# Optimization experiments

Measured on AMD Instinct MI355X. Metric: run time of the kernel, lower is better.

The kernel has to match this reference:

```python
import jax, jax.numpy as jnp
import numpy as np

OUT_F, IN_F = 4096, 4096
TOKENS = 8192


def setup_inputs() -> dict:
    key = jax.random.key(0)
    k0, k1, k2, k3 = jax.random.split(key, 4)
    CORE_SCALE = 0.05  # keep reconstructed W finite and well below the 1e6 sanity bound
    x = jax.random.normal(k0, (TOKENS, IN_F), dtype=jnp.float32)
    core0 = jax.random.normal(k1, (1, 16, 16, 64), dtype=jnp.float32) * CORE_SCALE
    core1 = jax.random.normal(k2, (64, 16, 16, 64), dtype=jnp.float32) * CORE_SCALE
    core2 = jax.random.normal(k3, (64, 16, 16, 1), dtype=jnp.float32) * CORE_SCALE
    return {"x": x, "core0": core0, "core1": core1, "core2": core2}


def _build_weight(cores):
    # Chain tensordot over bond dims: cores[k] is [r_{k-1}, o_k, i_k, r_k]
    t = cores[0].astype(jnp.float32)
    for c in cores[1:]:
        t = jnp.tensordot(t, c.astype(jnp.float32), axes=((-1,), (0,)))
    # squeeze the boundary bonds (both 1 for open boundary)
    t = t[0, ..., 0]  # shape [o1, i1, o2, i2, o3, i3]
    num = len(cores)
    # order 'oi': all o-axes first, then all i-axes (matches _contract_4d_chain_with)
    perm = list(range(0, 2 * num, 2)) + list(range(1, 2 * num, 2))
    t = jnp.transpose(t, perm)
    W = t.reshape(OUT_F, IN_F)
    # _clean_finite: nan/inf -> 0 (identity on finite values)
    return jnp.nan_to_num(W, nan=0.0, posinf=0.0, neginf=0.0)


def reference(x, core0, core1, core2):
    W = _build_weight([core0, core1, core2])  # [out_f, in_f], fp32
    # dense path: y = x @ W^T (nn.Linear semantics, no bias)
    return jnp.matmul(x, W.T)
```

## Files before the change

kernel.cpp:

```cpp
#include <hip/hip_runtime.h>

typedef __attribute__((ext_vector_type(8))) short  s8v;
typedef __attribute__((ext_vector_type(8))) unsigned short us8;
typedef __attribute__((ext_vector_type(4))) unsigned short us4;
typedef __attribute__((ext_vector_type(4))) float  f4v;

__device__ __forceinline__ unsigned short f2bf(float f) {
  unsigned int u = __builtin_bit_cast(unsigned int, f);
  u += 0x7fffu + ((u >> 16) & 1u);
  return (unsigned short)(u >> 16);
}

__device__ __forceinline__ void gll16(const void* g, void* l) {
  __builtin_amdgcn_global_load_lds(
      (const __attribute__((address_space(1))) unsigned int*)g,
      (__attribute__((address_space(3))) unsigned int*)l, 16, 0, 0);
}

__global__ __launch_bounds__(256) void cast_bf16(const float* __restrict__ in,
                                                 unsigned short* __restrict__ out) {
  const size_t i = (size_t)blockIdx.x * 256 + threadIdx.x;
  const f4v* p = (const f4v*)in;
  f4v a = p[2 * i];
  f4v b = p[2 * i + 1];
  us8 r;
  r[0] = f2bf(a[0]); r[1] = f2bf(a[1]); r[2] = f2bf(a[2]); r[3] = f2bf(a[3]);
  r[4] = f2bf(b[0]); r[5] = f2bf(b[1]); r[6] = f2bf(b[2]); r[7] = f2bf(b[3]);
  *(us8*)&out[i * 8] = r;
}

__global__ __launch_bounds__(256) void contract1b(const float* __restrict__ c0,
                                                  const float* __restrict__ c1,
                                                  unsigned short* __restrict__ T) {
  const int idx = blockIdx.x * 256 + threadIdx.x;
  const int r2q = idx & 15;
  const int oi2 = (idx >> 4) & 255;
  const int oi1 = idx >> 12;
  const float* c0p = c0 + oi1 * 64;
  const float* c1p = c1 + oi2 * 64 + r2q * 4;
  f4v s = (f4v)0.f;
#pragma unroll 8
  for (int r1 = 0; r1 < 64; ++r1) {
    const float t = c0p[r1];
    const f4v v = *(const f4v*)(c1p + r1 * 16384);
    s[0] = fmaf(t, v[0], s[0]); s[1] = fmaf(t, v[1], s[1]);
    s[2] = fmaf(t, v[2], s[2]); s[3] = fmaf(t, v[3], s[3]);
  }
  us4 o;
  o[0] = f2bf(s[0]); o[1] = f2bf(s[1]); o[2] = f2bf(s[2]); o[3] = f2bf(s[3]);
  *(us4*)&T[(size_t)idx * 4] = o;
}

__global__ __launch_bounds__(256) void transc2(const float* __restrict__ c2,
                                               unsigned short* __restrict__ c2t) {
  const int n = blockIdx.x * 16 + (threadIdx.x >> 4);
  const int j = threadIdx.x & 15;
  us4 o;
#pragma unroll
  for (int q = 0; q < 4; ++q) o[q] = f2bf(c2[(j * 4 + q) * 256 + n]);
  *(us4*)&c2t[(size_t)n * 64 + j * 4] = o;
}

__global__ __launch_bounds__(256) void buildW3(const unsigned short* __restrict__ T,
                                               const unsigned short* __restrict__ c2t,
                                               unsigned short* __restrict__ W) {
  __shared__ unsigned short sT[16384];
  __shared__ unsigned short sC[16384];

  const int tid = threadIdx.x;
  const int o1 = blockIdx.x >> 4, o2 = blockIdx.x & 15;

#pragma unroll
  for (int j = 0; j < 8; ++j) {
    const int c = j * 256 + tid;
    const int m = c >> 3, sl = c & 7;
    const int dst = m * 64 + ((sl ^ (m & 7)) << 3);
    *(us8*)&sT[dst] = *(const us8*)(T + (size_t)(o1 * 16 + (m >> 4)) * 16384 +
                                    (o2 * 16 + (m & 15)) * 64 + sl * 8);
    *(us8*)&sC[dst] = *(const us8*)(c2t + (size_t)m * 64 + sl * 8);
  }
  __syncthreads();

  const int lane = tid & 63, wid = tid >> 6;
  const int fr = lane & 15, ks = lane >> 4;
  const int f7 = fr & 7;
  const int sx0 = ((ks ^ f7) << 3);
  const int sx1 = (((4 + ks) ^ f7) << 3);

  s8v a[4][2];
#pragma unroll
  for (int mi = 0; mi < 4; ++mi) {
    const unsigned short* p = &sT[(wid * 64 + mi * 16 + fr) * 64];
    a[mi][0] = *(const s8v*)(p + sx0);
    a[mi][1] = *(const s8v*)(p + sx1);
  }
#pragma unroll
  for (int nt = 0; nt < 16; ++nt) {
    const unsigned short* p = &sC[(nt * 16 + fr) * 64];
    const s8v b0 = *(const s8v*)(p + sx0);
    const s8v b1 = *(const s8v*)(p + sx1);
#pragma unroll
    for (int mi = 0; mi < 4; ++mi) {
      f4v acc = (f4v)0.f;
      acc = __builtin_amdgcn_mfma_f32_16x16x32_bf16(a[mi][0], b0, acc, 0, 0, 0);
      acc = __builtin_amdgcn_mfma_f32_16x16x32_bf16(a[mi][1], b1, acc, 0, 0, 0);
      unsigned short* wp = W + (size_t)(o1 * 256 + o2 * 16 + nt) * 4096 +
                           (wid * 4 + mi) * 256 + fr;
#pragma unroll
      for (int r = 0; r < 4; ++r) wp[(ks * 4 + r) * 16] = f2bf(acc[r]);
    }
  }
}


#define SBAR() do { asm volatile("" ::: "memory"); __builtin_amdgcn_s_barrier(); asm volatile("" ::: "memory"); } while (0)
#define VMW(N) asm volatile("s_waitcnt vmcnt(" #N ")" ::: "memory")

template<int MQ, int NQ>
__device__ __forceinline__ void mmq(f4v (&acc)[8][4], const s8v (&a)[4][2], const s8v (&b)[2][2]) {
  __builtin_amdgcn_s_setprio(1);
#pragma unroll
  for (int mi = 0; mi < 4; ++mi)
#pragma unroll
    for (int ni = 0; ni < 2; ++ni)
#pragma unroll
      for (int q = 0; q < 2; ++q)
        acc[MQ * 4 + mi][NQ * 2 + ni] = __builtin_amdgcn_mfma_f32_16x16x32_bf16(
            a[mi][q], b[ni][q], acc[MQ * 4 + mi][NQ * 2 + ni], 0, 0, 0);
  __builtin_amdgcn_s_setprio(0);
}

__global__ __launch_bounds__(512, 2) void gemm8(const unsigned short* __restrict__ A,
                                                const unsigned short* __restrict__ B,
                                                float* __restrict__ C) {
  constexpr int N = 4096, K = 4096;
  constexpr int NT = K / 64;
  constexpr int NITER = NT / 2;
  constexpr int NXT = N / 256;

  __shared__ unsigned short lds[65536];

  const int tid  = threadIdx.x;
  const int lane = tid & 63;
  const int wid  = tid >> 6;
  const int wm   = wid >> 2;
  const int wn   = wid & 3;

  const int cpx = (int)gridDim.x >> 3;
  const int wg  = ((int)blockIdx.x & 7) * cpx + ((int)blockIdx.x >> 3);
  const long bm = (long)(wg / NXT) * 256;
  const long bn = (long)(wg % NXT) * 256;

  const int srow = tid >> 3;
  const int scol = ((tid & 7) ^ (srow & 7)) * 8;
  const unsigned short* gA = A + (bm + srow) * (size_t)K + scol;
  const unsigned short* gB = B + (bn + srow) * (size_t)K + scol;
  const size_t half64 = 64 * (size_t)K;
  const size_t k128   = 128 * (size_t)K;

#define STG(gp, koff, ldsU) do {                                  \
    const unsigned short* g_ = (gp) + (koff);                     \
    gll16(g_,          &lds[(ldsU) + tid * 8]);                   \
    gll16(g_ + half64, &lds[(ldsU) + 4096 + tid * 8]);            \
  } while (0)

  const int fr = lane & 15;
  const int ks = lane >> 4;
  const int f7 = fr & 7;
  const int sx0 = (ks ^ f7) * 8;
  const int sx1 = ((ks | 4) ^ f7) * 8;
  const int arow = (wm * 64 + fr) * 64;
  const int brow = (wn * 32 + fr) * 64;

#define RDA(MQ, bufU) do {                                                   \
    const unsigned short* p_ = &lds[(bufU) + (MQ) * 8192 + arow];            \
    a[0][0] = *(const s8v*)(p_ + sx0);        a[0][1] = *(const s8v*)(p_ + sx1); \
    a[1][0] = *(const s8v*)(p_ + 1024 + sx0); a[1][1] = *(const s8v*)(p_ + 1024 + sx1); \
    a[2][0] = *(const s8v*)(p_ + 2048 + sx0); a[2][1] = *(const s8v*)(p_ + 2048 + sx1); \
    a[3][0] = *(const s8v*)(p_ + 3072 + sx0); a[3][1] = *(const s8v*)(p_ + 3072 + sx1); \
  } while (0)
#define RDB(dst, NQ, bufU) do {                                              \
    const unsigned short* p_ = &lds[(bufU) + 16384 + (NQ) * 8192 + brow];    \
    dst[0][0] = *(const s8v*)(p_ + sx0);        dst[0][1] = *(const s8v*)(p_ + sx1); \
    dst[1][0] = *(const s8v*)(p_ + 1024 + sx0); dst[1][1] = *(const s8v*)(p_ + 1024 + sx1); \
  } while (0)

  f4v acc[8][4];
#pragma unroll
  for (int m = 0; m < 8; ++m)
#pragma unroll
    for (int n = 0; n < 4; ++n) acc[m][n] = (f4v)0.0f;

  STG(gA,        0, 0);
  STG(gA + k128, 0, 8192);
  STG(gB,        0, 16384);
  STG(gB + k128, 0, 24576);
  STG(gA,        64, 32768);
  VMW(2);
  SBAR();

  s8v a[4][2], bL[2][2], bH[2][2];

  for (int i = 0; i < NITER; ++i) {
    const long w46 = (i == NITER - 1) ? -128L : 0L;
    const long w8  = (i == NITER - 1) ? -192L : 0L;
    RDA(0, 0); RDB(bL, 0, 0); RDB(bH, 1, 0);
    STG(gB, 64, 32768 + 16384);
    SBAR(); mmq<0, 0>(acc, a, bL);
    STG(gA + k128, 64, 32768 + 8192);
    STG(gB + k128, 64, 32768 + 24576);
    SBAR(); mmq<0, 1>(acc, a, bH);
    RDA(1, 0);
    SBAR(); mmq<1, 0>(acc, a, bL);
    STG(gA, 128 + w46, 0);
    SBAR(); mmq<1, 1>(acc, a, bH);
    VMW(2); SBAR();
    RDA(0, 32768); RDB(bL, 0, 32768); RDB(bH, 1, 32768);
    STG(gB, 128 + w46, 16384);
    SBAR(); mmq<0, 0>(acc, a, bL);
    STG(gA + k128, 128 + w46, 8192);
    STG(gB + k128, 128 + w46, 24576);
    SBAR(); mmq<0, 1>(acc, a, bH);
    RDA(1, 32768);
    SBAR(); mmq<1, 0>(acc, a, bL);
    STG(gA, 192 + w8, 32768);
    SBAR(); mmq<1, 1>(acc, a, bH);
    VMW(2); SBAR();

    gA += 128; gB += 128;
  }
  VMW(0);

#pragma unroll
  for (int mq = 0; mq < 2; ++mq)
#pragma unroll
    for (int mi = 0; mi < 4; ++mi)
#pragma unroll
      for (int nq = 0; nq < 2; ++nq)
#pragma unroll
        for (int ni = 0; ni < 2; ++ni) {
          const size_t row0 = bm + mq * 128 + wm * 64 + mi * 16 + ks * 4;
          const size_t col  = bn + nq * 128 + wn * 32 + ni * 16 + fr;
          float* cp = C + row0 * (size_t)N + col;
          f4v v = acc[mq * 4 + mi][nq * 2 + ni];
          cp[0] = v[0]; cp[N] = v[1]; cp[2 * (size_t)N] = v[2]; cp[3 * (size_t)N] = v[3];
        }
#undef STG
#undef RDA
#undef RDB
}

extern "C" void kernel_launch(void* const* d_in, const int* in_sizes, int n_in,
                              void* d_out, int out_size, void* d_ws, size_t ws_size,
                              hipStream_t stream) {
  const float* x  = (const float*)d_in[0];
  const float* c0 = (const float*)d_in[1];
  const float* c1 = (const float*)d_in[2];
  const float* c2 = (const float*)d_in[3];
  float* out = (float*)d_out;

  char* ws = (char*)d_ws;
  unsigned short* T   = (unsigned short*)ws;
  unsigned short* c2t = (unsigned short*)(ws + (8u << 20));
  unsigned short* Wb  = (unsigned short*)(ws + (16u << 20));
  unsigned short* xb  = (unsigned short*)(ws + (48u << 20));

  hipLaunchKernelGGL(cast_bf16,  dim3(16384), dim3(256), 0, stream, x, xb);
  hipLaunchKernelGGL(contract1b, dim3(4096),  dim3(256), 0, stream, c0, c1, T);
  hipLaunchKernelGGL(transc2,    dim3(16),    dim3(256), 0, stream, c2, c2t);
  hipLaunchKernelGGL(buildW3,    dim3(256),   dim3(256), 0, stream, T, c2t, Wb);
  hipLaunchKernelGGL(gemm8,      dim3(512),   dim3(512), 0, stream, xb, Wb, out);
}
```

Measured before the change: 306.9 us.

## Compute first core contraction as bf16 MFMA GEMM instead of scalar FMA loop

```diff
diff --git a/kernel.cpp b/kernel.cpp
--- a/kernel.cpp
+++ b/kernel.cpp
@@ -29,26 +29,108 @@
   *(us8*)&out[i * 8] = r;
 }
 
-__global__ __launch_bounds__(256) void contract1b(const float* __restrict__ c0,
-                                                  const float* __restrict__ c1,
-                                                  unsigned short* __restrict__ T) {
-  const int idx = blockIdx.x * 256 + threadIdx.x;
-  const int r2q = idx & 15;
-  const int oi2 = (idx >> 4) & 255;
-  const int oi1 = idx >> 12;
-  const float* c0p = c0 + oi1 * 64;
-  const float* c1p = c1 + oi2 * 64 + r2q * 4;
-  f4v s = (f4v)0.f;
-#pragma unroll 8
-  for (int r1 = 0; r1 < 64; ++r1) {
-    const float t = c0p[r1];
-    const f4v v = *(const f4v*)(c1p + r1 * 16384);
-    s[0] = fmaf(t, v[0], s[0]); s[1] = fmaf(t, v[1], s[1]);
-    s[2] = fmaf(t, v[2], s[2]); s[3] = fmaf(t, v[3], s[3]);
-  }
-  us4 o;
-  o[0] = f2bf(s[0]); o[1] = f2bf(s[1]); o[2] = f2bf(s[2]); o[3] = f2bf(s[3]);
-  *(us4*)&T[(size_t)idx * 4] = o;
+__global__ __launch_bounds__(256) void cast_c0(const float* __restrict__ in,
+                                               unsigned short* __restrict__ out) {
+  const size_t i = (size_t)blockIdx.x * 256 + threadIdx.x;
+  const f4v* p = (const f4v*)in;
+  f4v a = p[2 * i];
+  f4v b = p[2 * i + 1];
+  us8 r;
+  r[0] = f2bf(a[0]); r[1] = f2bf(a[1]); r[2] = f2bf(a[2]); r[3] = f2bf(a[3]);
+  r[4] = f2bf(b[0]); r[5] = f2bf(b[1]); r[6] = f2bf(b[2]); r[7] = f2bf(b[3]);
+  *(us8*)&out[i * 8] = r;
+}
+
+__global__ __launch_bounds__(256) void tc1(const float* __restrict__ c1,
+                                           unsigned short* __restrict__ c1t) {
+  __shared__ float Tl[16384];
+  const int tid = threadIdx.x;
+  const int nb  = blockIdx.x;
+#pragma unroll
+  for (int j = 0; j < 16; ++j) {
+    const int c = j * 256 + tid;
+    const int k = c >> 6, nq = c & 63;
+    *(f4v*)&Tl[k * 256 + nq * 4] =
+        *(const f4v*)(c1 + (size_t)k * 16384 + nb * 256 + nq * 4);
+  }
+  __syncthreads();
+  const int nn = tid;
+  unsigned short* dst = c1t + (size_t)(nb * 256 + nn) * 64;
+#pragma unroll
+  for (int kq = 0; kq < 16; ++kq) {
+    us4 o;
+#pragma unroll
+    for (int r = 0; r < 4; ++r) o[r] = f2bf(Tl[(kq * 4 + r) * 256 + nn]);
+    *(us4*)&dst[kq * 4] = o;
+  }
+}
+
+__global__ __launch_bounds__(512) void tgemm(const unsigned short* __restrict__ c0bf,
+                                             const unsigned short* __restrict__ c1t,
+                                             unsigned short* __restrict__ T) {
+  __shared__ unsigned short sA[8192];
+  __shared__ unsigned short sB[16384];
+
+  const int tid = threadIdx.x;
+  const int nb = blockIdx.x, mb = blockIdx.y;
+
+#pragma unroll
+  for (int j = 0; j < 2; ++j) {
+    const int c = j * 512 + tid;
+    const int row = c >> 3, sl = c & 7;
+    *(us8*)&sA[row * 64 + ((sl ^ (row & 7)) << 3)] =
+        *(const us8*)(c0bf + (size_t)(mb * 128 + row) * 64 + sl * 8);
+  }
+#pragma unroll
+  for (int j = 0; j < 4; ++j) {
+    const int c = j * 512 + tid;
+    const int row = c >> 3, sl = c & 7;
+    *(us8*)&sB[row * 64 + ((sl ^ (row & 7)) << 3)] =
+        *(const us8*)(c1t + (size_t)(nb * 256 + row) * 64 + sl * 8);
+  }
+  __syncthreads();
+
+  const int lane = tid & 63, wid = tid >> 6;
+  const int wm = wid >> 2, wn = wid & 3;
+  const int fr = lane & 15, ks = lane >> 4;
+  const int f7 = fr & 7;
+  const int sx0 = (ks ^ f7) * 8;
+  const int sx1 = ((ks | 4) ^ f7) * 8;
+
+  s8v a[4][2], b[4][2];
+#pragma unroll
+  for (int mi = 0; mi < 4; ++mi) {
+    const unsigned short* p = &sA[(wm * 64 + mi * 16 + fr) * 64];
+    a[mi][0] = *(const s8v*)(p + sx0);
+    a[mi][1] = *(const s8v*)(p + sx1);
+  }
+#pragma unroll
+  for (int ni = 0; ni < 4; ++ni) {
+    const unsigned short* p = &sB[(wn * 64 + ni * 16 + fr) * 64];
+    b[ni][0] = *(const s8v*)(p + sx0);
+    b[ni][1] = *(const s8v*)(p + sx1);
+  }
+
+  f4v acc[4][4];
+#pragma unroll
+  for (int mi = 0; mi < 4; ++mi)
+#pragma unroll
+    for (int ni = 0; ni < 4; ++ni) {
+      acc[mi][ni] = (f4v)0.f;
+      acc[mi][ni] = __builtin_amdgcn_mfma_f32_16x16x32_bf16(a[mi][0], b[ni][0], acc[mi][ni], 0, 0, 0);
+      acc[mi][ni] = __builtin_amdgcn_mfma_f32_16x16x32_bf16(a[mi][1], b[ni][1], acc[mi][ni], 0, 0, 0);
+    }
+
+#pragma unroll
+  for (int mi = 0; mi < 4; ++mi)
+#pragma unroll
+    for (int ni = 0; ni < 4; ++ni) {
+      const int row0 = mb * 128 + wm * 64 + mi * 16 + ks * 4;
+      const size_t col = (size_t)nb * 256 + wn * 64 + ni * 16 + fr;
+#pragma unroll
+      for (int r = 0; r < 4; ++r)
+        T[(size_t)(row0 + r) * 16384 + col] = f2bf(acc[mi][ni][r]);
+    }
 }
 
 __global__ __launch_bounds__(256) void transc2(const float* __restrict__ c2,
@@ -111,7 +193,6 @@
     }
   }
 }
-
 
 #define SBAR() do { asm volatile("" ::: "memory"); __builtin_amdgcn_s_barrier(); asm volatile("" ::: "memory"); } while (0)
 #define VMW(N) asm volatile("s_waitcnt vmcnt(" #N ")" ::: "memory")
@@ -260,14 +341,18 @@
   float* out = (float*)d_out;
 
   char* ws = (char*)d_ws;
-  unsigned short* T   = (unsigned short*)ws;
-  unsigned short* c2t = (unsigned short*)(ws + (8u << 20));
-  unsigned short* Wb  = (unsigned short*)(ws + (16u << 20));
-  unsigned short* xb  = (unsigned short*)(ws + (48u << 20));
-
-  hipLaunchKernelGGL(cast_bf16,  dim3(16384), dim3(256), 0, stream, x, xb);
-  hipLaunchKernelGGL(contract1b, dim3(4096),  dim3(256), 0, stream, c0, c1, T);
-  hipLaunchKernelGGL(transc2,    dim3(16),    dim3(256), 0, stream, c2, c2t);
-  hipLaunchKernelGGL(buildW3,    dim3(256),   dim3(256), 0, stream, T, c2t, Wb);
-  hipLaunchKernelGGL(gemm8,      dim3(512),   dim3(512), 0, stream, xb, Wb, out);
-}
+  unsigned short* T    = (unsigned short*)ws;
+  unsigned short* c2t  = (unsigned short*)(ws + (8u << 20));
+  unsigned short* c0bf = (unsigned short*)(ws + (8u << 20) + 65536);
+  unsigned short* c1t  = (unsigned short*)(ws + (9u << 20));
+  unsigned short* Wb   = (unsigned short*)(ws + (16u << 20));
+  unsigned short* xb   = (unsigned short*)(ws + (48u << 20));
+
+  hipLaunchKernelGGL(cast_bf16, dim3(16384), dim3(256), 0, stream, x, xb);
+  hipLaunchKernelGGL(cast_c0,   dim3(8),     dim3(256), 0, stream, c0, c0bf);
+  hipLaunchKernelGGL(tc1,       dim3(64),    dim3(256), 0, stream, c1, c1t);
+  hipLaunchKernelGGL(tgemm,     dim3(64, 2), dim3(512), 0, stream, c0bf, c1t, T);
+  hipLaunchKernelGGL(transc2,   dim3(16),    dim3(256), 0, stream, c2, c2t);
+  hipLaunchKernelGGL(buildW3,   dim3(256),   dim3(256), 0, stream, T, c2t, Wb);
+  hipLaunchKernelGGL(gemm8,     dim3(512),   dim3(512), 0, stream, xb, Wb, out);
+}
```

Measured after the change: 276.2 us. 1.11x faster.
